# Kernel tuning notes

Hardware: AMD Instinct MI355X
Metric: run time of the kernel (lower is better)

The kernel has to match this reference:

```python
import jax, jax.numpy as jnp
import numpy as np

DIM = 1024
HEADS = 16
HEAD_DIM = DIM // HEADS
SCALE = HEAD_DIM ** -0.5


def setup_inputs() -> dict:
    key = jax.random.key(0)
    k_x, k_qkv, k_ow, k_ob = jax.random.split(key, 4)
    B, N = 4, 2048
    x = jax.random.normal(k_x, (B, N, DIM), dtype=jnp.float32)
    # nn.Linear(dim, 3*dim, bias=False): weight [3*dim, dim]; we store transposed [dim, 3*dim]
    w_qkv = jax.random.normal(k_qkv, (DIM, 3 * DIM), dtype=jnp.float32) * (DIM ** -0.5)
    w_out = jax.random.normal(k_ow, (DIM, DIM), dtype=jnp.float32) * (DIM ** -0.5)
    b_out = jax.random.normal(k_ob, (DIM,), dtype=jnp.float32) * 0.01
    return {"x": x, "w_qkv": w_qkv, "w_out": w_out, "b_out": b_out}


def reference(x, w_qkv, w_out, b_out):
    B, N, D = x.shape
    H, hd = HEADS, HEAD_DIM
    qkv = x @ w_qkv                                  # [B, N, 3D]
    qkv = qkv.reshape(B, N, 3, H, hd).transpose(2, 0, 3, 1, 4)  # [3, B, H, N, hd]
    q, k, v = qkv[0], qkv[1], qkv[2]
    dots = jnp.einsum('bhnd,bhmd->bhnm', q, k) * SCALE  # [B, H, N, N]
    attn = jax.nn.softmax(dots, axis=-1)
    out = jnp.einsum('bhnm,bhmd->bhnd', attn, v)     # [B, H, N, hd]
    out = out.transpose(0, 2, 1, 3).reshape(B, N, D)
    return out @ w_out + b_out
```

## Files before the change

kernel.cpp:

```cpp
#include <hip/hip_runtime.h>
#include <hip/hip_bf16.h>

#define BSZ   4
#define NSEQ  2048
#define DIMM  1024
#define NHEAD 16
#define HD    64
#define N3    (3*DIMM)
#define MTOK  (BSZ*NSEQ)
#define SCALE 0.125f
#define CQ    0.18033688011112042f

typedef __attribute__((ext_vector_type(8))) short    short8;
typedef __attribute__((ext_vector_type(4))) short    short4v;
typedef __attribute__((ext_vector_type(2))) unsigned uint2v;
typedef __attribute__((ext_vector_type(8))) __bf16   bf16x8;
typedef __attribute__((ext_vector_type(4))) float    f32x4;

__device__ inline short f2bf(float f) {
    unsigned u = __builtin_bit_cast(unsigned, f);
    u += 0x7fffu + ((u >> 16) & 1u);
    return (short)(u >> 16);
}

__device__ inline unsigned pack_bf16(float a, float b) {
    unsigned ua = __builtin_bit_cast(unsigned, a) + 0x8000u;
    unsigned ub = __builtin_bit_cast(unsigned, b) + 0x8000u;
    return __builtin_amdgcn_perm(ub, ua, 0x07060302u);
}

__device__ inline float fast_exp2(float x) {
#if __has_builtin(__builtin_amdgcn_exp2f)
    return __builtin_amdgcn_exp2f(x);
#else
    return exp2f(x);
#endif
}

__device__ inline bf16x8 lds_frag(const short* p) {
    return __builtin_bit_cast(bf16x8, *(const short8*)p);
}

__device__ inline bf16x8 glb_frag(const short* p) {
    return __builtin_bit_cast(bf16x8, *(const short8*)p);
}

__device__ inline void gld_lds16(const short* g, short* l) {
    __builtin_amdgcn_global_load_lds(
        (const __attribute__((address_space(1))) void*)g,
        (__attribute__((address_space(3))) void*)l, 16, 0, 0);
}

__device__ inline void transpose_tile(const float* __restrict__ src,
                                      short* __restrict__ dst,
                                      int K, int N, int bx, int by, int tid)
{
    __shared__ float tile[32][33];
    const int n0 = bx * 32, k0 = by * 32;
    const int tx = tid & 31, ty = tid >> 5;
    #pragma unroll
    for (int i = 0; i < 4; ++i)
        tile[ty + i * 8][tx] = src[(size_t)(k0 + ty + i * 8) * N + n0 + tx];
    __syncthreads();
    #pragma unroll
    for (int i = 0; i < 4; ++i)
        dst[(size_t)(n0 + ty + i * 8) * K + k0 + tx] = f2bf(tile[tx][ty + i * 8]);
}

__global__ __launch_bounds__(256)
void prepass(const float* __restrict__ x, short* __restrict__ xb,
             const float* __restrict__ wqkv, short* __restrict__ wqkvT,
             const float* __restrict__ wout, short* __restrict__ woutT)
{
    const int b = blockIdx.x, tid = threadIdx.x;
    if (b < 4096) {
        int i = b * 256 + tid;
        float4 v0 = ((const float4*)x)[i * 2];
        float4 v1 = ((const float4*)x)[i * 2 + 1];
        short8 s = { f2bf(v0.x), f2bf(v0.y), f2bf(v0.z), f2bf(v0.w),
                     f2bf(v1.x), f2bf(v1.y), f2bf(v1.z), f2bf(v1.w) };
        ((short8*)xb)[i] = s;
    } else if (b < 7168) {
        int idx = b - 4096;
        transpose_tile(wqkv, wqkvT, DIMM, N3, idx % 96, idx / 96, tid);
    } else {
        int idx = b - 7168;
        transpose_tile(wout, woutT, DIMM, DIMM, idx & 31, idx >> 5, tid);
    }
}

#define GEMM_KLOOP(APTR, BPTR)                                                 \
    for (int k0 = 0; k0 < DIMM; k0 += 32) {                                    \
        _Pragma("unroll")                                                      \
        for (int j = 0; j < 2; ++j) {                                          \
            int c = j * 256 + tid;                                             \
            int r = c >> 2, jj = c & 3;                                        \
            int gc = jj ^ ((r >> 1) & 3);                                      \
            gld_lds16(APTR + (size_t)(row0 + r) * DIMM + k0 + gc * 8,          \
                      As + c * 8);                                             \
            gld_lds16(BPTR + (size_t)(col0 + r) * DIMM + k0 + gc * 8,         \
                      Bs + c * 8);                                             \
        }                                                                      \
        __syncthreads();                                                       \
        bf16x8 af[4], bfr[4];                                                  \
        _Pragma("unroll")                                                      \
        for (int mt = 0; mt < 4; ++mt) {                                       \
            int row = wm + mt * 16 + l16;                                      \
            af[mt] = lds_frag(&As[row * 32 + (quad ^ ((row >> 1) & 3)) * 8]);  \
        }                                                                      \
        _Pragma("unroll")                                                      \
        for (int nt = 0; nt < 4; ++nt) {                                       \
            int row = wn + nt * 16 + l16;                                      \
            bfr[nt] = lds_frag(&Bs[row * 32 + (quad ^ ((row >> 1) & 3)) * 8]); \
        }                                                                      \
        _Pragma("unroll")                                                      \
        for (int mt = 0; mt < 4; ++mt)                                         \
            _Pragma("unroll")                                                  \
            for (int nt = 0; nt < 4; ++nt)                                     \
                acc[mt][nt] = __builtin_amdgcn_mfma_f32_16x16x32_bf16(         \
                    af[mt], bfr[nt], acc[mt][nt], 0, 0, 0);                    \
        __syncthreads();                                                       \
    }

__global__ __launch_bounds__(256, 2)
void gemm_qkv(const short* __restrict__ a, const short* __restrict__ bt,
              short* __restrict__ qo, short* __restrict__ ko,
              short* __restrict__ vo)
{
    __shared__ short As[128 * 32];
    __shared__ short Bs[128 * 32];
    const int tid  = threadIdx.x;
    const int wave = tid >> 6, lane = tid & 63;
    const int quad = lane >> 4, l16 = lane & 15;
    const int id   = blockIdx.x;
    const int xcd  = id & 7, j = id >> 3;
    const int jc   = j - (j / 3) * 3;
    const int row0 = (j / 3) * 128;
    const int col0 = (xcd * 3 + jc) * 128;
    const int wm = (wave >> 1) * 64, wn = (wave & 1) * 64;

    f32x4 acc[4][4] = {};
    GEMM_KLOOP(a, bt)

    #pragma unroll
    for (int mt = 0; mt < 4; ++mt) {
        #pragma unroll
        for (int nt = 0; nt < 4; ++nt) {
            int gcol  = col0 + wn + nt * 16 + l16;
            int which = gcol >> 10;
            int cc    = gcol & 1023;
            int h     = cc >> 6, d = cc & 63;
            int growb = row0 + wm + mt * 16 + quad * 4;
            int b_    = growb >> 11;
            int n_    = growb & 2047;
            int bh    = b_ * NHEAD + h;
            if (which == 2) {
                short4v s = { f2bf(acc[mt][nt][0]), f2bf(acc[mt][nt][1]),
                              f2bf(acc[mt][nt][2]), f2bf(acc[mt][nt][3]) };
                *(short4v*)(vo + ((size_t)bh * HD + d) * NSEQ + n_) = s;
            } else if (which == 0) {
                #pragma unroll
                for (int r = 0; r < 4; ++r)
                    qo[((size_t)bh * NSEQ + n_ + r) * HD + d] =
                        f2bf(acc[mt][nt][r] * CQ);
            } else {
                #pragma unroll
                for (int r = 0; r < 4; ++r)
                    ko[((size_t)bh * NSEQ + n_ + r) * HD + d] = f2bf(acc[mt][nt][r]);
            }
        }
    }
}

__global__ __launch_bounds__(256, 3)
void attn(const short* __restrict__ q, const short* __restrict__ k,
          const short* __restrict__ vt, short* __restrict__ o)
{
    __shared__ short Ks[2][64 * 64];
    __shared__ short Ps[4][32 * 72];

    const int tid  = threadIdx.x;
    const int wave = tid >> 6, lane = tid & 63;
    const int quad = lane >> 4, l16 = lane & 15;
    const int id   = blockIdx.x;
    const int xcd  = id & 7, j = id >> 3;
    const int bh   = xcd * 8 + (j >> 4);
    const int q0   = (j & 15) * 128;
    const size_t qkbase = (size_t)bh * NSEQ * HD;
    const size_t vbase  = (size_t)bh * HD * NSEQ;

    bf16x8 qf[2][2];
    #pragma unroll
    for (int g = 0; g < 2; ++g)
        #pragma unroll
        for (int ks = 0; ks < 2; ++ks)
            qf[g][ks] = glb_frag(q + qkbase +
                (size_t)(q0 + wave * 32 + g * 16 + l16) * HD + ks * 32 + quad * 8);

    f32x4 oacc[4][2] = {};
    float lsum[2] = {0.f, 0.f};
    short* Pw = &Ps[wave][0];

    const int  sr   = tid >> 3, sj = tid & 7;
    const int  soff = sr * HD + ((sj ^ (sr & 7)) * 8);
    const short* kbh = k + qkbase;

    gld_lds16(kbh + soff,            &Ks[0][tid * 8]);
    gld_lds16(kbh + soff + 32 * HD,  &Ks[0][2048 + tid * 8]);

    for (int t = 0; t < NSEQ / 64; ++t) {
        const int kv0 = t * 64;
        __syncthreads();
        if (t + 1 < NSEQ / 64) {
            const short* src = kbh + (size_t)(kv0 + 64) * HD;
            short* dst = &Ks[(t + 1) & 1][0];
            gld_lds16(src + soff,           dst + tid * 8);
            gld_lds16(src + soff + 32 * HD, dst + 2048 + tid * 8);
        }
        const short* Kb = &Ks[t & 1][0];

        bf16x8 vf[2][4];
        #pragma unroll
        for (int ks2 = 0; ks2 < 2; ++ks2)
            #pragma unroll
            for (int ot = 0; ot < 4; ++ot)
                vf[ks2][ot] = glb_frag(vt + vbase +
                    (size_t)(ot * 16 + l16) * NSEQ + kv0 + ks2 * 32 + quad * 8);

        f32x4 sacc[4][2] = {};
        #pragma unroll
        for (int nt = 0; nt < 4; ++nt) {
            int row = nt * 16 + l16;
            #pragma unroll
            for (int ks = 0; ks < 2; ++ks) {
                bf16x8 kf = lds_frag(&Kb[row * 64 + (((ks * 4 + quad) ^ (row & 7)) * 8)]);
                #pragma unroll
                for (int g = 0; g < 2; ++g)
                    sacc[nt][g] = __builtin_amdgcn_mfma_f32_16x16x32_bf16(
                        kf, qf[g][ks], sacc[nt][g], 0, 0, 0);
            }
        }

        #pragma unroll
        for (int g = 0; g < 2; ++g) {
            #pragma unroll
            for (int nt = 0; nt < 4; ++nt) {
                float p0 = fast_exp2(sacc[nt][g][0]);
                float p1 = fast_exp2(sacc[nt][g][1]);
                float p2 = fast_exp2(sacc[nt][g][2]);
                float p3 = fast_exp2(sacc[nt][g][3]);
                lsum[g] += (p0 + p1) + (p2 + p3);
                uint2v u = { pack_bf16(p0, p1), pack_bf16(p2, p3) };
                *(uint2v*)&Pw[(g * 16 + l16) * 72 + nt * 16 + quad * 4] = u;
            }
        }

        #pragma unroll
        for (int ks2 = 0; ks2 < 2; ++ks2) {
            bf16x8 pf[2];
            #pragma unroll
            for (int g = 0; g < 2; ++g)
                pf[g] = lds_frag(&Pw[(g * 16 + l16) * 72 + ks2 * 32 + quad * 8]);
            #pragma unroll
            for (int ot = 0; ot < 4; ++ot)
                #pragma unroll
                for (int g = 0; g < 2; ++g)
                    oacc[ot][g] = __builtin_amdgcn_mfma_f32_16x16x32_bf16(
                        vf[ks2][ot], pf[g], oacc[ot][g], 0, 0, 0);
        }
    }

    const int b_ = bh >> 4, h = bh & 15;
    float inv[2];
    #pragma unroll
    for (int g = 0; g < 2; ++g) {
        float l = lsum[g];
        l += __shfl_xor(l, 16);
        l += __shfl_xor(l, 32);
        inv[g] = 1.f / l;
    }
    #pragma unroll
    for (int ot = 0; ot < 4; ++ot) {
        #pragma unroll
        for (int g = 0; g < 2; ++g) {
            short4v s4 = { f2bf(oacc[ot][g][0] * inv[g]),
                           f2bf(oacc[ot][g][1] * inv[g]),
                           f2bf(oacc[ot][g][2] * inv[g]),
                           f2bf(oacc[ot][g][3] * inv[g]) };
            *(short4v*)(o + ((size_t)b_ * NSEQ + q0 + wave * 32 + g * 16 + l16) * DIMM +
                        h * HD + ot * 16 + quad * 4) = s4;
        }
    }
}

__global__ __launch_bounds__(256, 3)
void gemm_out(const short* __restrict__ a, const short* __restrict__ bt,
              const float* __restrict__ bias, float* __restrict__ out)
{
    __shared__ short As[64 * 32];
    __shared__ short Bs[128 * 32];
    const int tid  = threadIdx.x;
    const int wave = tid >> 6, lane = tid & 63;
    const int quad = lane >> 4, l16 = lane & 15;
    const int id   = blockIdx.x;
    const int row0 = (id >> 3) * 64, col0 = (id & 7) * 128;
    const int wm = (wave & 1) * 32, wn = (wave >> 1) * 64;

    f32x4 acc[2][4] = {};

    for (int k0 = 0; k0 < DIMM; k0 += 32) {
        {
            int r = tid >> 2, jj = tid & 3;
            int gc = jj ^ ((r >> 1) & 3);
            gld_lds16(a + (size_t)(row0 + r) * DIMM + k0 + gc * 8, As + tid * 8);
        }
        #pragma unroll
        for (int j = 0; j < 2; ++j) {
            int c = j * 256 + tid;
            int r = c >> 2, jj = c & 3;
            int gc = jj ^ ((r >> 1) & 3);
            gld_lds16(bt + (size_t)(col0 + r) * DIMM + k0 + gc * 8, Bs + c * 8);
        }
        __syncthreads();
        bf16x8 af[2], bfr[4];
        #pragma unroll
        for (int mt = 0; mt < 2; ++mt) {
            int row = wm + mt * 16 + l16;
            af[mt] = lds_frag(&As[row * 32 + (quad ^ ((row >> 1) & 3)) * 8]);
        }
        #pragma unroll
        for (int nt = 0; nt < 4; ++nt) {
            int row = wn + nt * 16 + l16;
            bfr[nt] = lds_frag(&Bs[row * 32 + (quad ^ ((row >> 1) & 3)) * 8]);
        }
        #pragma unroll
        for (int mt = 0; mt < 2; ++mt)
            #pragma unroll
            for (int nt = 0; nt < 4; ++nt)
                acc[mt][nt] = __builtin_amdgcn_mfma_f32_16x16x32_bf16(
                    af[mt], bfr[nt], acc[mt][nt], 0, 0, 0);
        __syncthreads();
    }

    #pragma unroll
    for (int mt = 0; mt < 2; ++mt) {
        #pragma unroll
        for (int nt = 0; nt < 4; ++nt) {
            int gcol = col0 + wn + nt * 16 + l16;
            float bb = bias[gcol];
            #pragma unroll
            for (int r = 0; r < 4; ++r) {
                int grow = row0 + wm + mt * 16 + quad * 4 + r;
                out[(size_t)grow * DIMM + gcol] = acc[mt][nt][r] + bb;
            }
        }
    }
}

extern "C" void kernel_launch(void* const* d_in, const int* in_sizes, int n_in,
                              void* d_out, int out_size, void* d_ws, size_t ws_size,
                              hipStream_t stream)
{
    const float* x     = (const float*)d_in[0];
    const float* w_qkv = (const float*)d_in[1];
    const float* w_out = (const float*)d_in[2];
    const float* b_out = (const float*)d_in[3];
    float* out = (float*)d_out;

    const size_t per = (size_t)BSZ * NHEAD * NSEQ * HD;
    short* q     = (short*)d_ws;
    short* kk    = q  + per;
    short* v     = kk + per;
    short* xb_ob = v  + per;
    short* wqkvT = xb_ob + per;
    short* woutT = wqkvT + (size_t)N3 * DIMM;

    prepass<<<8192, 256, 0, stream>>>(x, xb_ob, w_qkv, wqkvT, w_out, woutT);
    gemm_qkv<<<1536, 256, 0, stream>>>(xb_ob, wqkvT, q, kk, v);
    attn<<<1024, 256, 0, stream>>>(q, kk, v, xb_ob);
    gemm_out<<<1024, 256, 0, stream>>>(xb_ob, woutT, b_out, out);
}
```

Before: 320.1 us.

## Halve attention query tile per block to raise occupancy and grid size

```diff
diff --git a/kernel.cpp b/kernel.cpp
--- a/kernel.cpp
+++ b/kernel.cpp
@@ -172,34 +172,33 @@
     }
 }
 
-__global__ __launch_bounds__(256, 3)
+__global__ __launch_bounds__(256, 5)
 void attn(const short* __restrict__ q, const short* __restrict__ k,
           const short* __restrict__ vt, short* __restrict__ o)
 {
     __shared__ short Ks[2][64 * 64];
-    __shared__ short Ps[4][32 * 72];
+    __shared__ short Ps[4][16 * 72];
 
     const int tid  = threadIdx.x;
     const int wave = tid >> 6, lane = tid & 63;
     const int quad = lane >> 4, l16 = lane & 15;
     const int id   = blockIdx.x;
     const int xcd  = id & 7, j = id >> 3;
-    const int bh   = xcd * 8 + (j >> 4);
-    const int q0   = (j & 15) * 128;
+    const int bh   = xcd * 8 + (j >> 5);
+    const int q0   = (j & 31) * 64;
     const size_t qkbase = (size_t)bh * NSEQ * HD;
     const size_t vbase  = (size_t)bh * HD * NSEQ;
 
-    bf16x8 qf[2][2];
-    #pragma unroll
-    for (int g = 0; g < 2; ++g)
-        #pragma unroll
-        for (int ks = 0; ks < 2; ++ks)
-            qf[g][ks] = glb_frag(q + qkbase +
-                (size_t)(q0 + wave * 32 + g * 16 + l16) * HD + ks * 32 + quad * 8);
-
-    f32x4 oacc[4][2] = {};
-    float lsum[2] = {0.f, 0.f};
+    bf16x8 qf[2];
+    #pragma unroll
+    for (int ks = 0; ks < 2; ++ks)
+        qf[ks] = glb_frag(q + qkbase +
+            (size_t)(q0 + wave * 16 + l16) * HD + ks * 32 + quad * 8);
+
+    f32x4 oacc[4] = {};
+    float lsum = 0.f;
     short* Pw = &Ps[wave][0];
+    const short* vtb = vt + vbase + (size_t)l16 * NSEQ + quad * 8;
 
     const int  sr   = tid >> 3, sj = tid & 7;
     const int  soff = sr * HD + ((sj ^ (sr & 7)) * 8);
@@ -219,77 +218,64 @@
         }
         const short* Kb = &Ks[t & 1][0];
 
-        bf16x8 vf[2][4];
-        #pragma unroll
-        for (int ks2 = 0; ks2 < 2; ++ks2)
-            #pragma unroll
-            for (int ot = 0; ot < 4; ++ot)
-                vf[ks2][ot] = glb_frag(vt + vbase +
-                    (size_t)(ot * 16 + l16) * NSEQ + kv0 + ks2 * 32 + quad * 8);
-
-        f32x4 sacc[4][2] = {};
+        bf16x8 vf0[4];
+        #pragma unroll
+        for (int ot = 0; ot < 4; ++ot)
+            vf0[ot] = glb_frag(vtb + (size_t)(ot * 16) * NSEQ + kv0);
+
+        f32x4 sacc[4] = {};
         #pragma unroll
         for (int nt = 0; nt < 4; ++nt) {
             int row = nt * 16 + l16;
             #pragma unroll
             for (int ks = 0; ks < 2; ++ks) {
                 bf16x8 kf = lds_frag(&Kb[row * 64 + (((ks * 4 + quad) ^ (row & 7)) * 8)]);
-                #pragma unroll
-                for (int g = 0; g < 2; ++g)
-                    sacc[nt][g] = __builtin_amdgcn_mfma_f32_16x16x32_bf16(
-                        kf, qf[g][ks], sacc[nt][g], 0, 0, 0);
+                sacc[nt] = __builtin_amdgcn_mfma_f32_16x16x32_bf16(
+                    kf, qf[ks], sacc[nt], 0, 0, 0);
             }
         }
 
-        #pragma unroll
-        for (int g = 0; g < 2; ++g) {
-            #pragma unroll
-            for (int nt = 0; nt < 4; ++nt) {
-                float p0 = fast_exp2(sacc[nt][g][0]);
-                float p1 = fast_exp2(sacc[nt][g][1]);
-                float p2 = fast_exp2(sacc[nt][g][2]);
-                float p3 = fast_exp2(sacc[nt][g][3]);
-                lsum[g] += (p0 + p1) + (p2 + p3);
-                uint2v u = { pack_bf16(p0, p1), pack_bf16(p2, p3) };
-                *(uint2v*)&Pw[(g * 16 + l16) * 72 + nt * 16 + quad * 4] = u;
-            }
-        }
-
-        #pragma unroll
-        for (int ks2 = 0; ks2 < 2; ++ks2) {
-            bf16x8 pf[2];
-            #pragma unroll
-            for (int g = 0; g < 2; ++g)
-                pf[g] = lds_frag(&Pw[(g * 16 + l16) * 72 + ks2 * 32 + quad * 8]);
+        bf16x8 vf1[4];
+        #pragma unroll
+        for (int ot = 0; ot < 4; ++ot)
+            vf1[ot] = glb_frag(vtb + (size_t)(ot * 16) * NSEQ + kv0 + 32);
+
+        #pragma unroll
+        for (int nt = 0; nt < 4; ++nt) {
+            float p0 = fast_exp2(sacc[nt][0]);
+            float p1 = fast_exp2(sacc[nt][1]);
+            float p2 = fast_exp2(sacc[nt][2]);
+            float p3 = fast_exp2(sacc[nt][3]);
+            lsum += (p0 + p1) + (p2 + p3);
+            uint2v u = { pack_bf16(p0, p1), pack_bf16(p2, p3) };
+            *(uint2v*)&Pw[l16 * 72 + nt * 16 + quad * 4] = u;
+        }
+
+        {
+            bf16x8 pf0 = lds_frag(&Pw[l16 * 72 + quad * 8]);
             #pragma unroll
             for (int ot = 0; ot < 4; ++ot)
-                #pragma unroll
-                for (int g = 0; g < 2; ++g)
-                    oacc[ot][g] = __builtin_amdgcn_mfma_f32_16x16x32_bf16(
-                        vf[ks2][ot], pf[g], oacc[ot][g], 0, 0, 0);
+                oacc[ot] = __builtin_amdgcn_mfma_f32_16x16x32_bf16(
+                    vf0[ot], pf0, oacc[ot], 0, 0, 0);
+            bf16x8 pf1 = lds_frag(&Pw[l16 * 72 + 32 + quad * 8]);
+            #pragma unroll
+            for (int ot = 0; ot < 4; ++ot)
+                oacc[ot] = __builtin_amdgcn_mfma_f32_16x16x32_bf16(
+                    vf1[ot], pf1, oacc[ot], 0, 0, 0);
         }
     }
 
     const int b_ = bh >> 4, h = bh & 15;
-    float inv[2];
-    #pragma unroll
-    for (int g = 0; g < 2; ++g) {
-        float l = lsum[g];
-        l += __shfl_xor(l, 16);
-        l += __shfl_xor(l, 32);
-        inv[g] = 1.f / l;
-    }
+    float l = lsum;
+    l += __shfl_xor(l, 16);
+    l += __shfl_xor(l, 32);
+    float inv = 1.f / l;
     #pragma unroll
     for (int ot = 0; ot < 4; ++ot) {
-        #pragma unroll
-        for (int g = 0; g < 2; ++g) {
-            short4v s4 = { f2bf(oacc[ot][g][0] * inv[g]),
-                           f2bf(oacc[ot][g][1] * inv[g]),
-                           f2bf(oacc[ot][g][2] * inv[g]),
-                           f2bf(oacc[ot][g][3] * inv[g]) };
-            *(short4v*)(o + ((size_t)b_ * NSEQ + q0 + wave * 32 + g * 16 + l16) * DIMM +
-                        h * HD + ot * 16 + quad * 4) = s4;
-        }
+        short4v s4 = { f2bf(oacc[ot][0] * inv), f2bf(oacc[ot][1] * inv),
+                       f2bf(oacc[ot][2] * inv), f2bf(oacc[ot][3] * inv) };
+        *(short4v*)(o + ((size_t)b_ * NSEQ + q0 + wave * 16 + l16) * DIMM +
+                    h * HD + ot * 16 + quad * 4) = s4;
     }
 }
 
@@ -377,6 +363,6 @@
 
     prepass<<<8192, 256, 0, stream>>>(x, xb_ob, w_qkv, wqkvT, w_out, woutT);
     gemm_qkv<<<1536, 256, 0, stream>>>(xb_ob, wqkvT, q, kk, v);
-    attn<<<1024, 256, 0, stream>>>(q, kk, v, xb_ob);
+    attn<<<2048, 256, 0, stream>>>(q, kk, v, xb_ob);
     gemm_out<<<1024, 256, 0, stream>>>(xb_ob, woutT, b_out, out);
 }
```

Result: slower. 460.7 us (+43.9%).
